# Kernel optimization log

Measured on AMD Instinct MI355X. Metric: run time of the kernel, lower is better.

The kernel has to match this reference:

```python
import jax, jax.numpy as jnp
import numpy as np

N_STATIC = 20
N_DYNAMIC = 10
INPUT_DIM = N_STATIC + N_DYNAMIC * 9 + 8  # 118
EMBED = 128
HIDDEN = 1536
HIDDEN2 = 1024
OUT = 128
T = 2048


def setup_inputs() -> dict:
    key = jax.random.key(0)
    ks = jax.random.split(key, 20)
    s = lambda i, shape: jax.random.normal(ks[i], shape, dtype=jnp.float32) * 0.02
    inp = {
        "inputVecs": jax.random.normal(ks[0], (T, INPUT_DIM), dtype=jnp.float32),
        # init_hidden(): randn(num_layers, 1, hidden_dim) -> stored as [2, H]
        "h0": jax.random.normal(ks[1], (2, HIDDEN), dtype=jnp.float32),
        "c0": jax.random.normal(ks[2], (2, HIDDEN), dtype=jnp.float32),
        # LSTM layer 0 (input = INPUT_DIM + EMBED)
        "W_ih0": s(3, (4 * HIDDEN, INPUT_DIM + EMBED)),
        "W_hh0": s(4, (4 * HIDDEN, HIDDEN)),
        "b_ih0": s(5, (4 * HIDDEN,)),
        "b_hh0": s(6, (4 * HIDDEN,)),
        # LSTM layer 1
        "W_ih1": s(7, (4 * HIDDEN, HIDDEN)),
        "W_hh1": s(8, (4 * HIDDEN, HIDDEN)),
        "b_ih1": s(9, (4 * HIDDEN,)),
        "b_hh1": s(10, (4 * HIDDEN,)),
        # hiddenLinear: hidden_dim -> hidden2
        "W_hl": s(11, (HIDDEN2, HIDDEN)),
        "b_hl": s(12, (HIDDEN2,)),
        # linear: hidden2 -> output_dim
        "W_out": s(13, (OUT, HIDDEN2)),
        "b_out": s(14, (OUT,)),
        # map: output_dim -> embed_size
        "W_map": s(15, (EMBED, OUT)),
        "b_map": s(16, (EMBED,)),
    }
    return inp


def _lstm_cell(x, h, c, W_ih, W_hh, b_ih, b_hh):
    # torch gate order: i, f, g, o
    gates = W_ih @ x + b_ih + W_hh @ h + b_hh
    i, f, g, o = jnp.split(gates, 4)
    i = jax.nn.sigmoid(i)
    f = jax.nn.sigmoid(f)
    g = jnp.tanh(g)
    o = jax.nn.sigmoid(o)
    c_new = f * c + i * g
    h_new = o * jnp.tanh(c_new)
    return h_new, c_new


def reference(inputVecs, h0, c0, W_ih0, W_hh0, b_ih0, b_hh0,
              W_ih1, W_hh1, b_ih1, b_hh1,
              W_hl, b_hl, W_out, b_out, W_map, b_map):
    embed0 = jnp.zeros((EMBED,), dtype=inputVecs.dtype)

    def step(carry, x):
        h, c, emb = carry  # h,c: [2, H]; emb: [EMBED]
        xt = jnp.concatenate([x, emb])
        h0n, c0n = _lstm_cell(xt, h[0], c[0], W_ih0, W_hh0, b_ih0, b_hh0)
        h1n, c1n = _lstm_cell(h0n, h[1], c[1], W_ih1, W_hh1, b_ih1, b_hh1)
        # dropout p=0 -> identity; two stacked linears (no nonlinearity, faithful)
        y = W_out @ (W_hl @ h1n + b_hl) + b_out
        y = jax.nn.softmax(y)
        emb_new = W_map @ y + b_map
        return (jnp.stack([h0n, h1n]), jnp.stack([c0n, c1n]), emb_new), y

    _, outputs = jax.lax.scan(step, (h0, c0, embed0), inputVecs)
    return outputs  # [T, OUT]
```

## Files before the change

kernel.cpp:

```cpp
#include <hip/hip_runtime.h>
#include <math.h>
#include <stdint.h>

#define T_STEPS 2048
#define XDIM 118
#define EMBD 128
#define HD 1536
#define NA 96
#define NB 128
#define NBLK (NA + NB + 1)

#define SMEM_BYTES 160608

typedef uint32_t u32x4 __attribute__((ext_vector_type(4)));

struct Params {
  const float *x, *h0in, *c0in;
  const float *Wih0, *Whh0, *bih0, *bhh0;
  const float *Wih1, *Whh1, *bih1, *bhh1;
  const float *Whl, *bhl, *Wout, *bout;
  const float *Wfold;
  float *PRE, *Wc, *bc;
  uint4 *h0rec, *h1rec, *partrec, *yrec;
  float *out;
};

__device__ __forceinline__ float bf_lo(uint32_t u){ return __uint_as_float(u << 16); }
__device__ __forceinline__ float bf_hi(uint32_t u){ return __uint_as_float(u & 0xffff0000u); }
__device__ __forceinline__ uint32_t packbf(float a, float b){
  uint32_t ua = __float_as_uint(a), ub = __float_as_uint(b);
  ua = (ua + 0x7fffu + ((ua >> 16) & 1u)) >> 16;
  ub = (ub + 0x7fffu + ((ub >> 16) & 1u)) & 0xffff0000u;
  return (ua & 0xffffu) | ub;
}
__device__ __forceinline__ float sigm(float x){ return 1.f / (1.f + __expf(-x)); }

__device__ __forceinline__ u32x4 poll_rec(const uint4* p, uint32_t tag){
  u32x4 r; uint32_t n = 0;
  while (1){
    asm volatile("global_load_dwordx4 %0, %1, off sc0 sc1\n\ts_waitcnt vmcnt(0)"
                 : "=v"(r) : "v"(p) : "memory");
    if (r[2] >= tag) break;
    __builtin_amdgcn_s_sleep(2);
    if (++n > 2000000u) break;
  }
  return r;
}
__device__ __forceinline__ u32x4 rec_issue(const uint4* p){
  u32x4 r;
  asm volatile("global_load_dwordx4 %0, %1, off sc0 sc1" : "=v"(r) : "v"(p) : "memory");
  return r;
}
__device__ __forceinline__ void st_rec(uint4* p, float a, float b, uint32_t tag){
  u32x4 v; v[0] = __float_as_uint(a); v[1] = __float_as_uint(b); v[2] = tag; v[3] = 0u;
  asm volatile("global_store_dwordx4 %0, %1, off sc0 sc1" :: "v"(p), "v"(v) : "memory");
}

__device__ __forceinline__ float asrc(const Params& P, int r, int k){
  if (k < HD) return P.Whh0[(size_t)r * HD + k];
  return P.Wih0[(size_t)r * (XDIM + EMBD) + XDIM + (k - HD)];
}
__device__ void run_A(const Params& P, int bid, uint32_t* smem){
  const int tid = threadIdx.x;
  const int w = tid >> 6, l = tid & 63;
  const int O = bid * 16 + w;
  float* xv = (float*)smem;
  uint2* wl2 = (uint2*)(smem + 1664);
  float* h0loc = (float*)(smem + 18048);
  uint32_t wr[4][8];
  uint32_t wry[4];
#pragma unroll
  for (int g = 0; g < 4; ++g){
    int r = g * HD + O;
#pragma unroll
    for (int p = 0; p < 8; ++p)
      wr[g][p] = packbf(asrc(P, r, 128 * p + 2 * l), asrc(P, r, 128 * p + 2 * l + 1));
#pragma unroll
    for (int q = 0; q < 2; ++q){
      uint2 u;
      u.x = packbf(asrc(P, r, 128 * (8 + 2 * q) + 2 * l), asrc(P, r, 128 * (8 + 2 * q) + 2 * l + 1));
      u.y = packbf(asrc(P, r, 128 * (9 + 2 * q) + 2 * l), asrc(P, r, 128 * (9 + 2 * q) + 2 * l + 1));
      wl2[(q * 4 + g) * 1024 + tid] = u;
    }
    wry[g] = packbf(P.Wfold[(size_t)r * 128 + 2 * l], P.Wfold[(size_t)r * 128 + 2 * l + 1]);
  }
  float cst = P.c0in[O];
  __syncthreads();
  for (int t = 0; t < T_STEPS; ++t){
    const float* pre = P.PRE + (size_t)t * 6144;
    float q0 = pre[O], q1 = pre[HD + O], q2 = pre[2 * HD + O], q3 = pre[3 * HD + O];
    if (tid < 768){
      u32x4 r = poll_rec(P.h0rec + ((t & 1) ^ 1) * 768 + tid, (uint32_t)t);
      xv[2 * tid] = __uint_as_float(r[0]);
      xv[2 * tid + 1] = __uint_as_float(r[1]);
    }
    __syncthreads();
    float a0 = 0.f, a1 = 0.f, a2 = 0.f, a3 = 0.f;
#pragma unroll
    for (int p = 0; p < 8; ++p){
      float2 x2 = *(const float2*)&xv[128 * p + 2 * l];
      uint32_t u0 = wr[0][p], u1 = wr[1][p], u2 = wr[2][p], u3 = wr[3][p];
      a0 += bf_lo(u0) * x2.x + bf_hi(u0) * x2.y;
      a1 += bf_lo(u1) * x2.x + bf_hi(u1) * x2.y;
      a2 += bf_lo(u2) * x2.x + bf_hi(u2) * x2.y;
      a3 += bf_lo(u3) * x2.x + bf_hi(u3) * x2.y;
    }
#pragma unroll
    for (int q = 0; q < 2; ++q){
      float2 xa = *(const float2*)&xv[128 * (8 + 2 * q) + 2 * l];
      float2 xb = *(const float2*)&xv[128 * (9 + 2 * q) + 2 * l];
      uint2 u0 = wl2[(q * 4 + 0) * 1024 + tid];
      uint2 u1 = wl2[(q * 4 + 1) * 1024 + tid];
      uint2 u2 = wl2[(q * 4 + 2) * 1024 + tid];
      uint2 u3 = wl2[(q * 4 + 3) * 1024 + tid];
      a0 += bf_lo(u0.x) * xa.x + bf_hi(u0.x) * xa.y + bf_lo(u0.y) * xb.x + bf_hi(u0.y) * xb.y;
      a1 += bf_lo(u1.x) * xa.x + bf_hi(u1.x) * xa.y + bf_lo(u1.y) * xb.x + bf_hi(u1.y) * xb.y;
      a2 += bf_lo(u2.x) * xa.x + bf_hi(u2.x) * xa.y + bf_lo(u2.y) * xb.x + bf_hi(u2.y) * xb.y;
      a3 += bf_lo(u3.x) * xa.x + bf_hi(u3.x) * xa.y + bf_lo(u3.y) * xb.x + bf_hi(u3.y) * xb.y;
    }
    if (t > 0){
      u32x4 r = poll_rec(P.yrec + ((t & 1) ^ 1) * 64 + l, (uint32_t)t);
      float y0 = __uint_as_float(r[0]), y1 = __uint_as_float(r[1]);
      a0 += bf_lo(wry[0]) * y0 + bf_hi(wry[0]) * y1;
      a1 += bf_lo(wry[1]) * y0 + bf_hi(wry[1]) * y1;
      a2 += bf_lo(wry[2]) * y0 + bf_hi(wry[2]) * y1;
      a3 += bf_lo(wry[3]) * y0 + bf_hi(wry[3]) * y1;
    }
#pragma unroll
    for (int m = 1; m < 64; m <<= 1){
      a0 += __shfl_xor(a0, m, 64);
      a1 += __shfl_xor(a1, m, 64);
      a2 += __shfl_xor(a2, m, 64);
      a3 += __shfl_xor(a3, m, 64);
    }
    float gi = sigm(a0 + q0);
    float gf = sigm(a1 + q1);
    float gg = tanhf(a2 + q2);
    float go = sigm(a3 + q3);
    cst = gf * cst + gi * gg;
    float hn = go * tanhf(cst);
    if (l == 0) h0loc[w] = hn;
    __syncthreads();
    if (tid < 8)
      st_rec(P.h0rec + (t & 1) * 768 + bid * 8 + tid,
             h0loc[2 * tid], h0loc[2 * tid + 1], (uint32_t)(t + 1));
  }
}

__device__ __forceinline__ float bsrc(const Params& P, int r, int k){
  if (k < HD) return P.Wih1[(size_t)r * HD + k];
  return P.Whh1[(size_t)r * HD + (k - HD)];
}
__device__ void run_B(const Params& P, int bidb, uint32_t* smem){
  const int tid = threadIdx.x;
  const int w = tid >> 6, l = tid & 63;
  const int base = bidb * 12;
  float* xv = (float*)smem;
  uint2* wl2 = (uint2*)(smem + 3072);
  float* g1 = (float*)(smem + 39936);
  float* c1 = (float*)(smem + 39984);
  float* h1loc = (float*)(smem + 40008);
  float* plds = (float*)(smem + 40020);
  uint32_t wr[3][12];
  float bias[3];
#pragma unroll
  for (int jj = 0; jj < 3; ++jj){
    int idx = 3 * w + jj;
    int g = idx / 12, o = idx % 12;
    int r = g * HD + base + o;
    bias[jj] = P.bih1[r] + P.bhh1[r];
#pragma unroll
    for (int p = 0; p < 12; ++p)
      wr[jj][p] = packbf(bsrc(P, r, 128 * p + 2 * l), bsrc(P, r, 128 * p + 2 * l + 1));
#pragma unroll
    for (int q = 0; q < 6; ++q){
      uint2 u;
      u.x = packbf(bsrc(P, r, 128 * (12 + 2 * q) + 2 * l), bsrc(P, r, 128 * (12 + 2 * q) + 2 * l + 1));
      u.y = packbf(bsrc(P, r, 128 * (13 + 2 * q) + 2 * l), bsrc(P, r, 128 * (13 + 2 * q) + 2 * l + 1));
      wl2[(q * 3 + jj) * 1024 + tid] = u;
    }
  }
  const int jrow = tid >> 2, cpart = tid & 3;
  float wc0 = 0.f, wc1 = 0.f, wc2 = 0.f;
  if (tid < 512){
    const float* wcp = P.Wc + (size_t)jrow * HD + base + cpart * 3;
    wc0 = wcp[0]; wc1 = wcp[1]; wc2 = wcp[2];
  }
  if (tid < 12) c1[12 + tid] = P.c0in[HD + base + tid];
  __syncthreads();
  for (int t = 0; t < T_STEPS; ++t){
    if (tid < 768){
      u32x4 r = poll_rec(P.h1rec + ((t & 1) ^ 1) * 768 + tid, (uint32_t)t);
      xv[1536 + 2 * tid] = __uint_as_float(r[0]);
      xv[1537 + 2 * tid] = __uint_as_float(r[1]);
    }
    __syncthreads();
    float a0 = 0.f, a1 = 0.f, a2 = 0.f;
#pragma unroll
    for (int q = 0; q < 6; ++q){
      float2 xa = *(const float2*)&xv[128 * (12 + 2 * q) + 2 * l];
      float2 xb = *(const float2*)&xv[128 * (13 + 2 * q) + 2 * l];
      uint2 u0 = wl2[(q * 3 + 0) * 1024 + tid];
      uint2 u1 = wl2[(q * 3 + 1) * 1024 + tid];
      uint2 u2 = wl2[(q * 3 + 2) * 1024 + tid];
      a0 += bf_lo(u0.x) * xa.x + bf_hi(u0.x) * xa.y + bf_lo(u0.y) * xb.x + bf_hi(u0.y) * xb.y;
      a1 += bf_lo(u1.x) * xa.x + bf_hi(u1.x) * xa.y + bf_lo(u1.y) * xb.x + bf_hi(u1.y) * xb.y;
      a2 += bf_lo(u2.x) * xa.x + bf_hi(u2.x) * xa.y + bf_lo(u2.y) * xb.x + bf_hi(u2.y) * xb.y;
    }
    if (tid < 768){
      u32x4 r = poll_rec(P.h0rec + (t & 1) * 768 + tid, (uint32_t)(t + 1));
      xv[2 * tid] = __uint_as_float(r[0]);
      xv[2 * tid + 1] = __uint_as_float(r[1]);
    }
    __syncthreads();
#pragma unroll
    for (int p = 0; p < 12; ++p){
      float2 x2 = *(const float2*)&xv[128 * p + 2 * l];
      uint32_t u0 = wr[0][p], u1 = wr[1][p], u2 = wr[2][p];
      a0 += bf_lo(u0) * x2.x + bf_hi(u0) * x2.y;
      a1 += bf_lo(u1) * x2.x + bf_hi(u1) * x2.y;
      a2 += bf_lo(u2) * x2.x + bf_hi(u2) * x2.y;
    }
#pragma unroll
    for (int m = 1; m < 64; m <<= 1){
      a0 += __shfl_xor(a0, m, 64);
      a1 += __shfl_xor(a1, m, 64);
      a2 += __shfl_xor(a2, m, 64);
    }
    if (l == 0){
      g1[3 * w + 0] = a0 + bias[0];
      g1[3 * w + 1] = a1 + bias[1];
      g1[3 * w + 2] = a2 + bias[2];
    }
    __syncthreads();
    const int par = ((t & 1) ^ 1) * 12, cur = (t & 1) * 12;
    if (tid < 512){
      float h[3], cc[3];
#pragma unroll
      for (int ii = 0; ii < 3; ++ii){
        int o = cpart * 3 + ii;
        float gi = sigm(g1[o]);
        float gf = sigm(g1[12 + o]);
        float gg = tanhf(g1[24 + o]);
        float go = sigm(g1[36 + o]);
        float c = gf * c1[par + o] + gi * gg;
        cc[ii] = c;
        h[ii] = go * tanhf(c);
      }
      float pp = wc0 * h[0] + wc1 * h[1] + wc2 * h[2];
      pp += __shfl_xor(pp, 1, 64);
      pp += __shfl_xor(pp, 2, 64);
      if (cpart == 0) plds[jrow] = pp;
      if (jrow == 0){
#pragma unroll
        for (int ii = 0; ii < 3; ++ii){
          int o = cpart * 3 + ii;
          c1[cur + o] = cc[ii];
          h1loc[o] = h[ii];
        }
      }
    }
    __syncthreads();
    uint32_t tg = (uint32_t)(t + 1);
    if (tid < 6)
      st_rec(P.h1rec + (t & 1) * 768 + bidb * 6 + tid,
             h1loc[2 * tid], h1loc[2 * tid + 1], tg);
    else if (tid >= 64 && tid < 128){
      int r = tid - 64;
      st_rec(P.partrec + (size_t)(t & 1) * 8192 + bidb * 64 + r,
             plds[2 * r], plds[2 * r + 1], tg);
    }
  }
}

__device__ void run_C(const Params& P, uint32_t* smem){
  const int tid = threadIdx.x;
  float* partred = (float*)smem;
  float* bcs = (float*)(smem + 2048);
  const int w = tid >> 6, l = tid & 63;
  const int g8 = tid >> 6, j2 = tid & 63;
  if (tid < 128) bcs[tid] = P.bc[tid];
  __syncthreads();
  for (int t = 0; t < T_STEPS; ++t){
    const uint4* base = P.partrec + (size_t)(t & 1) * 8192;
    uint32_t tg = (uint32_t)(t + 1);
    u32x4 rec[8];
    uint32_t done = 0, n = 0;
    while (done != 0xFFu){
#pragma unroll
      for (int k = 0; k < 8; ++k)
        if (!(done & (1u << k))) rec[k] = rec_issue(base + (size_t)(8 * g8 + k) * 64 + j2);
      asm volatile("s_waitcnt vmcnt(0)" ::: "memory");
      __builtin_amdgcn_sched_barrier(0);
#pragma unroll
      for (int k = 0; k < 8; ++k)
        if (rec[k][2] >= tg) done |= (1u << k);
      if (done != 0xFFu){
        __builtin_amdgcn_s_sleep(2);
        if (++n > 2000000u) break;
      }
    }
    float s0 = 0.f, s1 = 0.f;
#pragma unroll
    for (int k = 0; k < 8; ++k){
      s0 += __uint_as_float(rec[k][0]);
      s1 += __uint_as_float(rec[k][1]);
    }
    partred[g8 * 128 + 2 * j2] = s0;
    partred[g8 * 128 + 2 * j2 + 1] = s1;
    __syncthreads();
    if (w == 0){
      float lt0 = bcs[2 * l], lt1 = bcs[2 * l + 1];
#pragma unroll
      for (int g = 0; g < 16; ++g){
        lt0 += partred[g * 128 + 2 * l];
        lt1 += partred[g * 128 + 2 * l + 1];
      }
      float m = fmaxf(lt0, lt1);
#pragma unroll
      for (int k = 1; k < 64; k <<= 1) m = fmaxf(m, __shfl_xor(m, k, 64));
      float e0 = __expf(lt0 - m), e1 = __expf(lt1 - m);
      float sd = e0 + e1;
#pragma unroll
      for (int k = 1; k < 64; k <<= 1) sd += __shfl_xor(sd, k, 64);
      float inv = 1.f / sd;
      float y0 = e0 * inv, y1 = e1 * inv;
      P.out[(size_t)t * 128 + 2 * l] = y0;
      P.out[(size_t)t * 128 + 2 * l + 1] = y1;
      st_rec(P.yrec + (t & 1) * 64 + l, y0, y1, tg);
    }
  }
}

__global__ __launch_bounds__(1024) void k_lstm(Params P){
  extern __shared__ __align__(16) uint32_t smem[];
  int bid = blockIdx.x;
  if (bid < NA) run_A(P, bid, smem);
  else if (bid < NA + NB) run_B(P, bid - NA, smem);
  else run_C(P, smem);
}

__global__ void k_init(const float* h0in, uint4* h0rec, uint4* h1rec,
                       uint4* partrec, uint4* yrec){
  int tid = threadIdx.x;
  for (int i = tid; i < 768; i += 256){
    uint4 r0; r0.x = __float_as_uint(h0in[2 * i]); r0.y = __float_as_uint(h0in[2 * i + 1]);
    r0.z = 0u; r0.w = 0u;
    h0rec[i] = r0; h0rec[768 + i] = r0;
    uint4 r1; r1.x = __float_as_uint(h0in[HD + 2 * i]); r1.y = __float_as_uint(h0in[HD + 2 * i + 1]);
    r1.z = 0u; r1.w = 0u;
    h1rec[i] = r1; h1rec[768 + i] = r1;
  }
  uint4 z; z.x = 0u; z.y = 0u; z.z = 0u; z.w = 0u;
  for (int i = tid; i < 16384; i += 256) partrec[i] = z;
  for (int i = tid; i < 128; i += 256) yrec[i] = z;
}

__global__ void k_fold(const float* Wih0, const float* Wmap, const float* bmap,
                       float* Wfold, float* bfold){
  __shared__ float we[64 * 128];
  int b = blockIdx.x, tid = threadIdx.x;
  int r0 = b * 64;
  for (int i = tid; i < 64 * 128; i += 256){
    int rr = i >> 7, e = i & 127;
    we[i] = Wih0[(size_t)(r0 + rr) * (XDIM + EMBD) + XDIM + e];
  }
  __syncthreads();
  int j = tid & 127, half = tid >> 7;
  float acc[32];
#pragma unroll
  for (int rr = 0; rr < 32; ++rr) acc[rr] = 0.f;
  for (int e = 0; e < 128; ++e){
    float wv = Wmap[(size_t)e * 128 + j];
#pragma unroll
    for (int rr = 0; rr < 32; ++rr) acc[rr] += we[(half * 32 + rr) * 128 + e] * wv;
  }
  for (int rr = 0; rr < 32; ++rr)
    Wfold[(size_t)(r0 + half * 32 + rr) * 128 + j] = acc[rr];
  if (tid < 64){
    float a = 0.f;
    for (int e = 0; e < 128; ++e) a += we[tid * 128 + e] * bmap[e];
    bfold[r0 + tid] = a;
  }
}

__global__ void k_pre(const float* x, const float* Wih0, const float* bih0, const float* bhh0,
                      const float* bfold, float* PRE){
  int tb = blockIdx.x >> 2;
  int rc = blockIdx.x & 3;
  int tid = threadIdx.x;
  __shared__ float xl[32 * XDIM];
  for (int i = tid; i < 32 * XDIM; i += 256){
    int tt = i / XDIM, k = i % XDIM;
    xl[i] = x[(size_t)(tb * 32 + tt) * XDIM + k];
  }
  __syncthreads();
  for (int rr = 0; rr < 6; ++rr){
    int r = rc * HD + rr * 256 + tid;
    float acc[32];
#pragma unroll
    for (int t = 0; t < 32; ++t) acc[t] = 0.f;
    const float* wrow = Wih0 + (size_t)r * (XDIM + EMBD);
    for (int k = 0; k < XDIM; ++k){
      float wv = wrow[k];
#pragma unroll
      for (int t = 0; t < 32; ++t) acc[t] += wv * xl[t * XDIM + k];
    }
    float bb = bih0[r] + bhh0[r];
    float bf = bfold[r];
    for (int t = 0; t < 32; ++t)
      PRE[(size_t)(tb * 32 + t) * 6144 + r] = acc[t] + bb + ((tb * 32 + t) > 0 ? bf : 0.f);
  }
}

__global__ void k_wc(const float* Whl, const float* Wout, const float* bhl, const float* bout,
                     float* Wc, float* bc){
  if (blockIdx.x == 96){
    int j = threadIdx.x;
    if (j < 128){
      float a = 0.f;
      for (int m = 0; m < 1024; ++m) a += Wout[(size_t)j * 1024 + m] * bhl[m];
      bc[j] = a + bout[j];
    }
    return;
  }
  int kt = blockIdx.x % 6, jt = blockIdx.x / 6;
  __shared__ float wo[8 * 1024];
  int tid = threadIdx.x;
  for (int i = tid; i < 8 * 1024; i += 256) wo[i] = Wout[(size_t)(jt * 8) * 1024 + i];
  __syncthreads();
  int k = kt * 256 + tid;
  float acc[8];
#pragma unroll
  for (int jj = 0; jj < 8; ++jj) acc[jj] = 0.f;
  for (int m = 0; m < 1024; ++m){
    float wl = Whl[(size_t)m * HD + k];
#pragma unroll
    for (int jj = 0; jj < 8; ++jj) acc[jj] += wo[jj * 1024 + m] * wl;
  }
#pragma unroll
  for (int jj = 0; jj < 8; ++jj) Wc[(size_t)(jt * 8 + jj) * HD + k] = acc[jj];
}

__global__ void k_sentinel(float* out){ out[0] = 1.0e6f; }

extern "C" void kernel_launch(void* const* d_in, const int* in_sizes, int n_in,
                              void* d_out, int out_size, void* d_ws, size_t ws_size,
                              hipStream_t stream){
  (void)in_sizes; (void)n_in; (void)out_size;
  const float* x    = (const float*)d_in[0];
  const float* h0in = (const float*)d_in[1];
  const float* c0in = (const float*)d_in[2];
  const float* Wih0 = (const float*)d_in[3];
  const float* Whh0 = (const float*)d_in[4];
  const float* bih0 = (const float*)d_in[5];
  const float* bhh0 = (const float*)d_in[6];
  const float* Wih1 = (const float*)d_in[7];
  const float* Whh1 = (const float*)d_in[8];
  const float* bih1 = (const float*)d_in[9];
  const float* bhh1 = (const float*)d_in[10];
  const float* Whl  = (const float*)d_in[11];
  const float* bhl  = (const float*)d_in[12];
  const float* Wout = (const float*)d_in[13];
  const float* bout = (const float*)d_in[14];
  const float* Wmap = (const float*)d_in[15];
  const float* bmap = (const float*)d_in[16];
  float* out = (float*)d_out;
  float* ws = (float*)d_ws;

  size_t off = 0;
  float* PRE    = ws + off; off += (size_t)T_STEPS * 6144;
  float* Wc     = ws + off; off += 128 * HD;
  float* bc     = ws + off; off += 128;
  float* Wfold  = ws + off; off += (size_t)6144 * 128;
  float* bfold  = ws + off; off += 6144;
  off = (off + 3) & ~(size_t)3;
  uint4* h0rec   = (uint4*)(ws + off); off += 2 * 768 * 4;
  uint4* h1rec   = (uint4*)(ws + off); off += 2 * 768 * 4;
  uint4* partrec = (uint4*)(ws + off); off += 2 * 8192 * 4;
  uint4* yrec    = (uint4*)(ws + off); off += 2 * 64 * 4;

  if (ws_size < off * sizeof(float) + 1024){
    hipLaunchKernelGGL(k_sentinel, dim3(1), dim3(1), 0, stream, out);
    return;
  }

  (void)hipFuncSetAttribute(reinterpret_cast<const void*>(k_lstm),
                            hipFuncAttributeMaxDynamicSharedMemorySize, SMEM_BYTES);

  hipLaunchKernelGGL(k_init, dim3(1), dim3(256), 0, stream, h0in, h0rec, h1rec, partrec, yrec);
  hipLaunchKernelGGL(k_fold, dim3(96), dim3(256), 0, stream, Wih0, Wmap, bmap, Wfold, bfold);
  hipLaunchKernelGGL(k_pre, dim3(256), dim3(256), 0, stream, x, Wih0, bih0, bhh0, bfold, PRE);
  hipLaunchKernelGGL(k_wc, dim3(97), dim3(256), 0, stream, Whl, Wout, bhl, bout, Wc, bc);

  Params P;
  P.x = x; P.h0in = h0in; P.c0in = c0in;
  P.Wih0 = Wih0; P.Whh0 = Whh0; P.bih0 = bih0; P.bhh0 = bhh0;
  P.Wih1 = Wih1; P.Whh1 = Whh1; P.bih1 = bih1; P.bhh1 = bhh1;
  P.Whl = Whl; P.bhl = bhl; P.Wout = Wout; P.bout = bout;
  P.Wfold = Wfold;
  P.PRE = PRE; P.Wc = Wc; P.bc = bc;
  P.h0rec = h0rec; P.h1rec = h1rec; P.partrec = partrec; P.yrec = yrec;
  P.out = out;

  hipLaunchKernelGGL(k_lstm, dim3(NBLK), dim3(1024), SMEM_BYTES, stream, P);
}
```

Measured before the change: 27.81 ms.

## Replace per-record tagged polling with per-block tag flags and packed data buffers

Cross-block communication changes from tagged records, where every 16-byte record carries a tag and many threads poll, to dense float4 data buffers plus one tag word per producer block. A single wavefront polls all producer tags and releases the rest of the block through an LDS flag, then the data is read once without polling. Producers write data, wait for the stores to complete, then publish a tag. This cuts the global polling traffic and doubles the payload per record, at the cost of an extra store-ordering wait and LDS spin barriers. The memory-ordering correctness between data and tag visibility is the main risk.

```diff
diff --git a/kernel.cpp b/kernel.cpp
--- a/kernel.cpp
+++ b/kernel.cpp
@@ -13,6 +13,7 @@
 #define SMEM_BYTES 160608
 
 typedef uint32_t u32x4 __attribute__((ext_vector_type(4)));
+typedef uint32_t u32x2 __attribute__((ext_vector_type(2)));
 
 struct Params {
   const float *x, *h0in, *c0in;
@@ -21,7 +22,8 @@
   const float *Whl, *bhl, *Wout, *bout;
   const float *Wfold;
   float *PRE, *Wc, *bc;
-  uint4 *h0rec, *h1rec, *partrec, *yrec;
+  uint4 *h0dat, *h1dat, *partdat, *yrec;
+  uint32_t *atag, *btag;
   float *out;
 };
 
@@ -35,25 +37,69 @@
 }
 __device__ __forceinline__ float sigm(float x){ return 1.f / (1.f + __expf(-x)); }
 
+__device__ __forceinline__ u32x4 ld_rec(const uint4* p){
+  u32x4 r;
+  asm volatile("global_load_dwordx4 %0, %1, off sc0 sc1\n\ts_waitcnt vmcnt(0)"
+               : "=v"(r) : "v"(p) : "memory");
+  return r;
+}
+__device__ __forceinline__ void st_rec4(uint4* p, float4 d){
+  u32x4 v; v[0] = __float_as_uint(d.x); v[1] = __float_as_uint(d.y);
+  v[2] = __float_as_uint(d.z); v[3] = __float_as_uint(d.w);
+  asm volatile("global_store_dwordx4 %0, %1, off sc0 sc1" :: "v"(p), "v"(v) : "memory");
+}
+__device__ __forceinline__ void st_tag(uint32_t* p, uint32_t v){
+  asm volatile("global_store_dword %0, %1, off sc0 sc1" :: "v"(p), "v"(v) : "memory");
+}
 __device__ __forceinline__ u32x4 poll_rec(const uint4* p, uint32_t tag){
   u32x4 r; uint32_t n = 0;
   while (1){
     asm volatile("global_load_dwordx4 %0, %1, off sc0 sc1\n\ts_waitcnt vmcnt(0)"
                  : "=v"(r) : "v"(p) : "memory");
     if (r[2] >= tag) break;
-    __builtin_amdgcn_s_sleep(2);
+    __builtin_amdgcn_s_sleep(1);
     if (++n > 2000000u) break;
   }
   return r;
 }
-__device__ __forceinline__ u32x4 rec_issue(const uint4* p){
-  u32x4 r;
-  asm volatile("global_load_dwordx4 %0, %1, off sc0 sc1" : "=v"(r) : "v"(p) : "memory");
-  return r;
-}
-__device__ __forceinline__ void st_rec(uint4* p, float a, float b, uint32_t tag){
-  u32x4 v; v[0] = __float_as_uint(a); v[1] = __float_as_uint(b); v[2] = tag; v[3] = 0u;
-  asm volatile("global_store_dwordx4 %0, %1, off sc0 sc1" :: "v"(p), "v"(v) : "memory");
+__device__ __forceinline__ void poll_tags96(const uint32_t* tag, int l, uint32_t tgt){
+  uint32_t n = 0;
+  while (1){
+    uint32_t v0, v1;
+    asm volatile("global_load_dword %0, %2, off sc0 sc1\n\t"
+                 "global_load_dword %1, %3, off sc0 sc1\n\t"
+                 "s_waitcnt vmcnt(0)"
+                 : "=v"(v0), "=v"(v1)
+                 : "v"(tag + 4 * l), "v"(tag + 4 * (64 + (l & 31))) : "memory");
+    bool ok = (v0 >= tgt) && (l >= 32 || v1 >= tgt);
+    if (__all(ok)) break;
+    __builtin_amdgcn_s_sleep(1);
+    if (++n > 2000000u) break;
+  }
+}
+__device__ __forceinline__ void poll_tags128(const uint32_t* tag, int l, uint32_t tgt){
+  uint32_t n = 0;
+  while (1){
+    uint32_t v0, v1;
+    asm volatile("global_load_dword %0, %2, off sc0 sc1\n\t"
+                 "global_load_dword %1, %3, off sc0 sc1\n\t"
+                 "s_waitcnt vmcnt(0)"
+                 : "=v"(v0), "=v"(v1)
+                 : "v"(tag + 4 * l), "v"(tag + 4 * (64 + l)) : "memory");
+    if (__all(v0 >= tgt && v1 >= tgt)) break;
+    __builtin_amdgcn_s_sleep(1);
+    if (++n > 2000000u) break;
+  }
+}
+__device__ __forceinline__ void lds_set(volatile uint32_t* f, uint32_t v){
+  asm volatile("" ::: "memory");
+  *f = v;
+  asm volatile("" ::: "memory");
+}
+__device__ __forceinline__ void lds_wait(volatile uint32_t* f, uint32_t tgt){
+  uint32_t n = 0;
+  while (*f < tgt){ if (++n > 1000000000u) break; }
+  asm volatile("" ::: "memory");
 }
 
 __device__ __forceinline__ float asrc(const Params& P, int r, int k){
@@ -65,8 +111,10 @@
   const int w = tid >> 6, l = tid & 63;
   const int O = bid * 16 + w;
   float* xv = (float*)smem;
+  float* ybc = (float*)smem + 1536;
   uint2* wl2 = (uint2*)(smem + 1664);
   float* h0loc = (float*)(smem + 18048);
+  volatile uint32_t* flg = smem + 18064;
   uint32_t wr[4][8];
   uint32_t wry[4];
 #pragma unroll
@@ -85,14 +133,22 @@
     wry[g] = packbf(P.Wfold[(size_t)r * 128 + 2 * l], P.Wfold[(size_t)r * 128 + 2 * l + 1]);
   }
   float cst = P.c0in[O];
+  if (tid < 2) flg[tid] = 0u;
   __syncthreads();
   for (int t = 0; t < T_STEPS; ++t){
     const float* pre = P.PRE + (size_t)t * 6144;
     float q0 = pre[O], q1 = pre[HD + O], q2 = pre[2 * HD + O], q3 = pre[3 * HD + O];
-    if (tid < 768){
-      u32x4 r = poll_rec(P.h0rec + ((t & 1) ^ 1) * 768 + tid, (uint32_t)t);
-      xv[2 * tid] = __uint_as_float(r[0]);
-      xv[2 * tid + 1] = __uint_as_float(r[1]);
+    if (w == 0){
+      if (t > 0) poll_tags96(P.atag, l, (uint32_t)t);
+      lds_set(flg + 0, (uint32_t)t);
+    } else if (w < 6){
+      lds_wait(flg + 0, (uint32_t)t);
+    }
+    if (tid < 384){
+      u32x4 r = ld_rec(P.h0dat + ((t & 1) ^ 1) * 384 + tid);
+      float4 f; f.x = __uint_as_float(r[0]); f.y = __uint_as_float(r[1]);
+      f.z = __uint_as_float(r[2]); f.w = __uint_as_float(r[3]);
+      *(float4*)&xv[4 * tid] = f;
     }
     __syncthreads();
     float a0 = 0.f, a1 = 0.f, a2 = 0.f, a3 = 0.f;
@@ -119,8 +175,15 @@
       a3 += bf_lo(u3.x) * xa.x + bf_hi(u3.x) * xa.y + bf_lo(u3.y) * xb.x + bf_hi(u3.y) * xb.y;
     }
     if (t > 0){
-      u32x4 r = poll_rec(P.yrec + ((t & 1) ^ 1) * 64 + l, (uint32_t)t);
-      float y0 = __uint_as_float(r[0]), y1 = __uint_as_float(r[1]);
+      if (w == 0){
+        u32x4 r = poll_rec(P.yrec + ((t & 1) ^ 1) * 64 + l, (uint32_t)t);
+        ybc[2 * l] = __uint_as_float(r[0]);
+        ybc[2 * l + 1] = __uint_as_float(r[1]);
+        lds_set(flg + 1, (uint32_t)t);
+      } else {
+        lds_wait(flg + 1, (uint32_t)t);
+      }
+      float y0 = ybc[2 * l], y1 = ybc[2 * l + 1];
       a0 += bf_lo(wry[0]) * y0 + bf_hi(wry[0]) * y1;
       a1 += bf_lo(wry[1]) * y0 + bf_hi(wry[1]) * y1;
       a2 += bf_lo(wry[2]) * y0 + bf_hi(wry[2]) * y1;
@@ -141,9 +204,12 @@
     float hn = go * tanhf(cst);
     if (l == 0) h0loc[w] = hn;
     __syncthreads();
-    if (tid < 8)
-      st_rec(P.h0rec + (t & 1) * 768 + bid * 8 + tid,
-             h0loc[2 * tid], h0loc[2 * tid + 1], (uint32_t)(t + 1));
+    if (w == 0){
+      if (l < 4) st_rec4(P.h0dat + (t & 1) * 384 + bid * 4 + l,
+                         *(const float4*)&h0loc[4 * l]);
+      asm volatile("s_waitcnt vmcnt(0)" ::: "memory");
+      if (l == 0) st_tag(P.atag + 4 * bid, (uint32_t)(t + 1));
+    }
   }
 }
 
@@ -161,6 +227,7 @@
   float* c1 = (float*)(smem + 39984);
   float* h1loc = (float*)(smem + 40008);
   float* plds = (float*)(smem + 40020);
+  volatile uint32_t* flg = smem + 40148;
   uint32_t wr[3][12];
   float bias[3];
 #pragma unroll
@@ -187,12 +254,20 @@
     wc0 = wcp[0]; wc1 = wcp[1]; wc2 = wcp[2];
   }
   if (tid < 12) c1[12 + tid] = P.c0in[HD + base + tid];
+  if (tid < 2) flg[tid] = 0u;
   __syncthreads();
   for (int t = 0; t < T_STEPS; ++t){
-    if (tid < 768){
-      u32x4 r = poll_rec(P.h1rec + ((t & 1) ^ 1) * 768 + tid, (uint32_t)t);
-      xv[1536 + 2 * tid] = __uint_as_float(r[0]);
-      xv[1537 + 2 * tid] = __uint_as_float(r[1]);
+    if (w == 0){
+      if (t > 0) poll_tags128(P.btag, l, (uint32_t)t);
+      lds_set(flg + 0, (uint32_t)t);
+    } else if (w < 6){
+      lds_wait(flg + 0, (uint32_t)t);
+    }
+    if (tid < 384){
+      u32x4 r = ld_rec(P.h1dat + ((t & 1) ^ 1) * 384 + tid);
+      float4 f; f.x = __uint_as_float(r[0]); f.y = __uint_as_float(r[1]);
+      f.z = __uint_as_float(r[2]); f.w = __uint_as_float(r[3]);
+      *(float4*)&xv[1536 + 4 * tid] = f;
     }
     __syncthreads();
     float a0 = 0.f, a1 = 0.f, a2 = 0.f;
@@ -207,10 +282,17 @@
       a1 += bf_lo(u1.x) * xa.x + bf_hi(u1.x) * xa.y + bf_lo(u1.y) * xb.x + bf_hi(u1.y) * xb.y;
       a2 += bf_lo(u2.x) * xa.x + bf_hi(u2.x) * xa.y + bf_lo(u2.y) * xb.x + bf_hi(u2.y) * xb.y;
     }
-    if (tid < 768){
-      u32x4 r = poll_rec(P.h0rec + (t & 1) * 768 + tid, (uint32_t)(t + 1));
-      xv[2 * tid] = __uint_as_float(r[0]);
-      xv[2 * tid + 1] = __uint_as_float(r[1]);
+    if (w == 0){
+      poll_tags96(P.atag, l, (uint32_t)(t + 1));
+      lds_set(flg + 1, (uint32_t)(t + 1));
+    } else if (w < 6){
+      lds_wait(flg + 1, (uint32_t)(t + 1));
+    }
+    if (tid < 384){
+      u32x4 r = ld_rec(P.h0dat + (t & 1) * 384 + tid);
+      float4 f; f.x = __uint_as_float(r[0]); f.y = __uint_as_float(r[1]);
+      f.z = __uint_as_float(r[2]); f.w = __uint_as_float(r[3]);
+      *(float4*)&xv[4 * tid] = f;
     }
     __syncthreads();
 #pragma unroll
@@ -261,14 +343,17 @@
       }
     }
     __syncthreads();
-    uint32_t tg = (uint32_t)(t + 1);
-    if (tid < 6)
-      st_rec(P.h1rec + (t & 1) * 768 + bidb * 6 + tid,
-             h1loc[2 * tid], h1loc[2 * tid + 1], tg);
-    else if (tid >= 64 && tid < 128){
-      int r = tid - 64;
-      st_rec(P.partrec + (size_t)(t & 1) * 8192 + bidb * 64 + r,
-             plds[2 * r], plds[2 * r + 1], tg);
+    if (w == 1){
+      if (l < 32){
+        st_rec4(P.partdat + ((size_t)(t & 1) * 128 + bidb) * 32 + l,
+                *(const float4*)&plds[4 * l]);
+      } else if (l < 35){
+        int r = l - 32;
+        st_rec4(P.h1dat + (t & 1) * 384 + bidb * 3 + r,
+                *(const float4*)&h1loc[4 * r]);
+      }
+      asm volatile("s_waitcnt vmcnt(0)" ::: "memory");
+      if (l == 0) st_tag(P.btag + 4 * bidb, (uint32_t)(t + 1));
     }
   }
 }
@@ -276,43 +361,44 @@
 __device__ void run_C(const Params& P, uint32_t* smem){
   const int tid = threadIdx.x;
   float* partred = (float*)smem;
-  float* bcs = (float*)(smem + 2048);
+  float* bcs = (float*)(smem + 4096);
+  volatile uint32_t* flg = smem + 4224;
   const int w = tid >> 6, l = tid & 63;
-  const int g8 = tid >> 6, j2 = tid & 63;
+  const int s = tid & 31, bg = tid >> 5;
   if (tid < 128) bcs[tid] = P.bc[tid];
+  if (tid == 0) flg[0] = 0u;
   __syncthreads();
   for (int t = 0; t < T_STEPS; ++t){
-    const uint4* base = P.partrec + (size_t)(t & 1) * 8192;
     uint32_t tg = (uint32_t)(t + 1);
-    u32x4 rec[8];
-    uint32_t done = 0, n = 0;
-    while (done != 0xFFu){
-#pragma unroll
-      for (int k = 0; k < 8; ++k)
-        if (!(done & (1u << k))) rec[k] = rec_issue(base + (size_t)(8 * g8 + k) * 64 + j2);
-      asm volatile("s_waitcnt vmcnt(0)" ::: "memory");
-      __builtin_amdgcn_sched_barrier(0);
-#pragma unroll
-      for (int k = 0; k < 8; ++k)
-        if (rec[k][2] >= tg) done |= (1u << k);
-      if (done != 0xFFu){
-        __builtin_amdgcn_s_sleep(2);
-        if (++n > 2000000u) break;
-      }
-    }
-    float s0 = 0.f, s1 = 0.f;
-#pragma unroll
-    for (int k = 0; k < 8; ++k){
-      s0 += __uint_as_float(rec[k][0]);
-      s1 += __uint_as_float(rec[k][1]);
-    }
-    partred[g8 * 128 + 2 * j2] = s0;
-    partred[g8 * 128 + 2 * j2 + 1] = s1;
+    if (w == 0){
+      poll_tags128(P.btag, l, tg);
+      lds_set(flg, tg);
+    } else {
+      lds_wait(flg, tg);
+    }
+    {
+      const uint4* pb = P.partdat + ((size_t)(t & 1) * 128 + 4 * bg) * 32 + s;
+      u32x4 r0, r1, r2, r3;
+      asm volatile(
+        "global_load_dwordx4 %0, %4, off sc0 sc1\n\t"
+        "global_load_dwordx4 %1, %5, off sc0 sc1\n\t"
+        "global_load_dwordx4 %2, %6, off sc0 sc1\n\t"
+        "global_load_dwordx4 %3, %7, off sc0 sc1\n\t"
+        "s_waitcnt vmcnt(0)"
+        : "=v"(r0), "=v"(r1), "=v"(r2), "=v"(r3)
+        : "v"(pb), "v"(pb + 32), "v"(pb + 64), "v"(pb + 96) : "memory");
+      float4 acc;
+      acc.x = __uint_as_float(r0[0]) + __uint_as_float(r1[0]) + __uint_as_float(r2[0]) + __uint_as_float(r3[0]);
+      acc.y = __uint_as_float(r0[1]) + __uint_as_float(r1[1]) + __uint_as_float(r2[1]) + __uint_as_float(r3[1]);
+      acc.z = __uint_as_float(r0[2]) + __uint_as_float(r1[2]) + __uint_as_float(r2[2]) + __uint_as_float(r3[2]);
+      acc.w = __uint_as_float(r0[3]) + __uint_as_float(r1[3]) + __uint_as_float(r2[3]) + __uint_as_float(r3[3]);
+      *(float4*)&partred[bg * 128 + 4 * s] = acc;
+    }
     __syncthreads();
     if (w == 0){
       float lt0 = bcs[2 * l], lt1 = bcs[2 * l + 1];
 #pragma unroll
-      for (int g = 0; g < 16; ++g){
+      for (int g = 0; g < 32; ++g){
         lt0 += partred[g * 128 + 2 * l];
         lt1 += partred[g * 128 + 2 * l + 1];
       }
@@ -327,7 +413,9 @@
       float y0 = e0 * inv, y1 = e1 * inv;
       P.out[(size_t)t * 128 + 2 * l] = y0;
       P.out[(size_t)t * 128 + 2 * l + 1] = y1;
-      st_rec(P.yrec + (t & 1) * 64 + l, y0, y1, tg);
+      u32x4 v; v[0] = __float_as_uint(y0); v[1] = __float_as_uint(y1); v[2] = tg; v[3] = 0u;
+      uint4* yp = P.yrec + (t & 1) * 64 + l;
+      asm volatile("global_store_dwordx4 %0, %1, off sc0 sc1" :: "v"(yp), "v"(v) : "memory");
     }
   }
 }
@@ -340,20 +428,23 @@
   else run_C(P, smem);
 }
 
-__global__ void k_init(const float* h0in, uint4* h0rec, uint4* h1rec,
-                       uint4* partrec, uint4* yrec){
+__global__ void k_init(const float* h0in, uint4* h0dat, uint4* h1dat, uint4* yrec,
+                       uint32_t* atag, uint32_t* btag){
   int tid = threadIdx.x;
   for (int i = tid; i < 768; i += 256){
-    uint4 r0; r0.x = __float_as_uint(h0in[2 * i]); r0.y = __float_as_uint(h0in[2 * i + 1]);
-    r0.z = 0u; r0.w = 0u;
-    h0rec[i] = r0; h0rec[768 + i] = r0;
-    uint4 r1; r1.x = __float_as_uint(h0in[HD + 2 * i]); r1.y = __float_as_uint(h0in[HD + 2 * i + 1]);
-    r1.z = 0u; r1.w = 0u;
-    h1rec[i] = r1; h1rec[768 + i] = r1;
+    int r = i % 384;
+    uint4 v0, v1;
+    v0.x = __float_as_uint(h0in[4 * r]);     v0.y = __float_as_uint(h0in[4 * r + 1]);
+    v0.z = __float_as_uint(h0in[4 * r + 2]); v0.w = __float_as_uint(h0in[4 * r + 3]);
+    h0dat[i] = v0;
+    v1.x = __float_as_uint(h0in[HD + 4 * r]);     v1.y = __float_as_uint(h0in[HD + 4 * r + 1]);
+    v1.z = __float_as_uint(h0in[HD + 4 * r + 2]); v1.w = __float_as_uint(h0in[HD + 4 * r + 3]);
+    h1dat[i] = v1;
   }
   uint4 z; z.x = 0u; z.y = 0u; z.z = 0u; z.w = 0u;
-  for (int i = tid; i < 16384; i += 256) partrec[i] = z;
   for (int i = tid; i < 128; i += 256) yrec[i] = z;
+  for (int i = tid; i < 96 * 4; i += 256) atag[i] = 0u;
+  for (int i = tid; i < 128 * 4; i += 256) btag[i] = 0u;
 }
 
 __global__ void k_fold(const float* Wih0, const float* Wmap, const float* bmap,
@@ -474,11 +565,14 @@
   float* bc     = ws + off; off += 128;
   float* Wfold  = ws + off; off += (size_t)6144 * 128;
   float* bfold  = ws + off; off += 6144;
-  off = (off + 3) & ~(size_t)3;
-  uint4* h0rec   = (uint4*)(ws + off); off += 2 * 768 * 4;
-  uint4* h1rec   = (uint4*)(ws + off); off += 2 * 768 * 4;
-  uint4* partrec = (uint4*)(ws + off); off += 2 * 8192 * 4;
-  uint4* yrec    = (uint4*)(ws + off); off += 2 * 64 * 4;
+  off = (off + 31) & ~(size_t)31;
+  uint4* h0dat   = (uint4*)(ws + off); off += 768 * 4;
+  uint4* h1dat   = (uint4*)(ws + off); off += 768 * 4;
+  uint4* partdat = (uint4*)(ws + off); off += 2 * 128 * 32 * 4;
+  uint4* yrec    = (uint4*)(ws + off); off += 128 * 4;
+  uint32_t* atag = (uint32_t*)(ws + off); off += 96 * 4;
+  off = (off + 31) & ~(size_t)31;
+  uint32_t* btag = (uint32_t*)(ws + off); off += 128 * 4;
 
   if (ws_size < off * sizeof(float) + 1024){
     hipLaunchKernelGGL(k_sentinel, dim3(1), dim3(1), 0, stream, out);
@@ -488,7 +582,7 @@
   (void)hipFuncSetAttribute(reinterpret_cast<const void*>(k_lstm),
                             hipFuncAttributeMaxDynamicSharedMemorySize, SMEM_BYTES);
 
-  hipLaunchKernelGGL(k_init, dim3(1), dim3(256), 0, stream, h0in, h0rec, h1rec, partrec, yrec);
+  hipLaunchKernelGGL(k_init, dim3(1), dim3(256), 0, stream, h0in, h0dat, h1dat, yrec, atag, btag);
   hipLaunchKernelGGL(k_fold, dim3(96), dim3(256), 0, stream, Wih0, Wmap, bmap, Wfold, bfold);
   hipLaunchKernelGGL(k_pre, dim3(256), dim3(256), 0, stream, x, Wih0, bih0, bhh0, bfold, PRE);
   hipLaunchKernelGGL(k_wc, dim3(97), dim3(256), 0, stream, Whl, Wout, bhl, bout, Wc, bc);
@@ -500,7 +594,8 @@
   P.Whl = Whl; P.bhl = bhl; P.Wout = Wout; P.bout = bout;
   P.Wfold = Wfold;
   P.PRE = PRE; P.Wc = Wc; P.bc = bc;
-  P.h0rec = h0rec; P.h1rec = h1rec; P.partrec = partrec; P.yrec = yrec;
+  P.h0dat = h0dat; P.h1dat = h1dat; P.partdat = partdat; P.yrec = yrec;
+  P.atag = atag; P.btag = btag;
   P.out = out;
 
   hipLaunchKernelGGL(k_lstm, dim3(NBLK), dim3(1024), SMEM_BYTES, stream, P);
```

Result: slower. 37.61 ms (+35.3%).

## Publish one hidden value per record to drop per-step block barriers

Applied to the files above, without the earlier changes.

Each wave now writes its own hidden-state record (one float plus tag) straight to global memory, instead of gathering values in LDS behind a __syncthreads and storing pairs. Consumers poll two records per thread with both loads issued before a single wait. Layer-A's input buffer is double-buffered by step parity so the trailing barrier can be removed safely. Partial sums are also stored directly from shuffled registers. This shortens the cross-block critical path each timestep, at the cost of twice as many records to poll and more small stores.

```diff
diff --git a/kernel.cpp b/kernel.cpp
--- a/kernel.cpp
+++ b/kernel.cpp
@@ -46,6 +46,21 @@
   }
   return r;
 }
+__device__ __forceinline__ void poll2(const uint4* p0, const uint4* p1, uint32_t tag,
+                                      float* d0, float* d1){
+  u32x4 a, b; uint32_t n = 0;
+  while (1){
+    asm volatile("global_load_dwordx4 %0, %2, off sc0 sc1\n\t"
+                 "global_load_dwordx4 %1, %3, off sc0 sc1\n\t"
+                 "s_waitcnt vmcnt(0)"
+                 : "=v"(a), "=v"(b) : "v"(p0), "v"(p1) : "memory");
+    if (a[2] >= tag && b[2] >= tag) break;
+    __builtin_amdgcn_s_sleep(2);
+    if (++n > 2000000u) break;
+  }
+  *d0 = __uint_as_float(a[0]);
+  *d1 = __uint_as_float(b[0]);
+}
 __device__ __forceinline__ u32x4 rec_issue(const uint4* p){
   u32x4 r;
   asm volatile("global_load_dwordx4 %0, %1, off sc0 sc1" : "=v"(r) : "v"(p) : "memory");
@@ -64,9 +79,7 @@
   const int tid = threadIdx.x;
   const int w = tid >> 6, l = tid & 63;
   const int O = bid * 16 + w;
-  float* xv = (float*)smem;
-  uint2* wl2 = (uint2*)(smem + 1664);
-  float* h0loc = (float*)(smem + 18048);
+  uint2* wl2 = (uint2*)(smem + 3072);
   uint32_t wr[4][8];
   uint32_t wry[4];
 #pragma unroll
@@ -89,10 +102,10 @@
   for (int t = 0; t < T_STEPS; ++t){
     const float* pre = P.PRE + (size_t)t * 6144;
     float q0 = pre[O], q1 = pre[HD + O], q2 = pre[2 * HD + O], q3 = pre[3 * HD + O];
+    float* xv = (float*)smem + (t & 1) * 1536;
     if (tid < 768){
-      u32x4 r = poll_rec(P.h0rec + ((t & 1) ^ 1) * 768 + tid, (uint32_t)t);
-      xv[2 * tid] = __uint_as_float(r[0]);
-      xv[2 * tid + 1] = __uint_as_float(r[1]);
+      const uint4* p = P.h0rec + ((t & 1) ^ 1) * 1536 + 2 * tid;
+      poll2(p, p + 1, (uint32_t)t, &xv[2 * tid], &xv[2 * tid + 1]);
     }
     __syncthreads();
     float a0 = 0.f, a1 = 0.f, a2 = 0.f, a3 = 0.f;
@@ -139,11 +152,7 @@
     float go = sigm(a3 + q3);
     cst = gf * cst + gi * gg;
     float hn = go * tanhf(cst);
-    if (l == 0) h0loc[w] = hn;
-    __syncthreads();
-    if (tid < 8)
-      st_rec(P.h0rec + (t & 1) * 768 + bid * 8 + tid,
-             h0loc[2 * tid], h0loc[2 * tid + 1], (uint32_t)(t + 1));
+    if (l == 0) st_rec(P.h0rec + (t & 1) * 1536 + O, hn, 0.f, (uint32_t)(t + 1));
   }
 }
 
@@ -159,8 +168,6 @@
   uint2* wl2 = (uint2*)(smem + 3072);
   float* g1 = (float*)(smem + 39936);
   float* c1 = (float*)(smem + 39984);
-  float* h1loc = (float*)(smem + 40008);
-  float* plds = (float*)(smem + 40020);
   uint32_t wr[3][12];
   float bias[3];
 #pragma unroll
@@ -190,9 +197,8 @@
   __syncthreads();
   for (int t = 0; t < T_STEPS; ++t){
     if (tid < 768){
-      u32x4 r = poll_rec(P.h1rec + ((t & 1) ^ 1) * 768 + tid, (uint32_t)t);
-      xv[1536 + 2 * tid] = __uint_as_float(r[0]);
-      xv[1537 + 2 * tid] = __uint_as_float(r[1]);
+      const uint4* p = P.h1rec + ((t & 1) ^ 1) * 1536 + 2 * tid;
+      poll2(p, p + 1, (uint32_t)t, &xv[1536 + 2 * tid], &xv[1537 + 2 * tid]);
     }
     __syncthreads();
     float a0 = 0.f, a1 = 0.f, a2 = 0.f;
@@ -208,9 +214,8 @@
       a2 += bf_lo(u2.x) * xa.x + bf_hi(u2.x) * xa.y + bf_lo(u2.y) * xb.x + bf_hi(u2.y) * xb.y;
     }
     if (tid < 768){
-      u32x4 r = poll_rec(P.h0rec + (t & 1) * 768 + tid, (uint32_t)(t + 1));
-      xv[2 * tid] = __uint_as_float(r[0]);
-      xv[2 * tid + 1] = __uint_as_float(r[1]);
+      const uint4* p = P.h0rec + (t & 1) * 1536 + 2 * tid;
+      poll2(p, p + 1, (uint32_t)(t + 1), &xv[2 * tid], &xv[2 * tid + 1]);
     }
     __syncthreads();
 #pragma unroll
@@ -234,6 +239,7 @@
     }
     __syncthreads();
     const int par = ((t & 1) ^ 1) * 12, cur = (t & 1) * 12;
+    uint32_t tg = (uint32_t)(t + 1);
     if (tid < 512){
       float h[3], cc[3];
 #pragma unroll
@@ -250,25 +256,17 @@
       float pp = wc0 * h[0] + wc1 * h[1] + wc2 * h[2];
       pp += __shfl_xor(pp, 1, 64);
       pp += __shfl_xor(pp, 2, 64);
-      if (cpart == 0) plds[jrow] = pp;
+      float pp2 = __shfl_xor(pp, 4, 64);
+      if ((tid & 7) == 0)
+        st_rec(P.partrec + (size_t)(t & 1) * 8192 + bidb * 64 + (tid >> 3), pp, pp2, tg);
       if (jrow == 0){
 #pragma unroll
         for (int ii = 0; ii < 3; ++ii){
           int o = cpart * 3 + ii;
           c1[cur + o] = cc[ii];
-          h1loc[o] = h[ii];
+          st_rec(P.h1rec + (t & 1) * 1536 + base + o, h[ii], 0.f, tg);
         }
       }
-    }
-    __syncthreads();
-    uint32_t tg = (uint32_t)(t + 1);
-    if (tid < 6)
-      st_rec(P.h1rec + (t & 1) * 768 + bidb * 6 + tid,
-             h1loc[2 * tid], h1loc[2 * tid + 1], tg);
-    else if (tid >= 64 && tid < 128){
-      int r = tid - 64;
-      st_rec(P.partrec + (size_t)(t & 1) * 8192 + bidb * 64 + r,
-             plds[2 * r], plds[2 * r + 1], tg);
     }
   }
 }
@@ -343,13 +341,11 @@
 __global__ void k_init(const float* h0in, uint4* h0rec, uint4* h1rec,
                        uint4* partrec, uint4* yrec){
   int tid = threadIdx.x;
-  for (int i = tid; i < 768; i += 256){
-    uint4 r0; r0.x = __float_as_uint(h0in[2 * i]); r0.y = __float_as_uint(h0in[2 * i + 1]);
-    r0.z = 0u; r0.w = 0u;
-    h0rec[i] = r0; h0rec[768 + i] = r0;
-    uint4 r1; r1.x = __float_as_uint(h0in[HD + 2 * i]); r1.y = __float_as_uint(h0in[HD + 2 * i + 1]);
-    r1.z = 0u; r1.w = 0u;
-    h1rec[i] = r1; h1rec[768 + i] = r1;
+  for (int i = tid; i < 1536; i += 256){
+    uint4 r0; r0.x = __float_as_uint(h0in[i]); r0.y = 0u; r0.z = 0u; r0.w = 0u;
+    h0rec[i] = r0; h0rec[1536 + i] = r0;
+    uint4 r1; r1.x = __float_as_uint(h0in[HD + i]); r1.y = 0u; r1.z = 0u; r1.w = 0u;
+    h1rec[i] = r1; h1rec[1536 + i] = r1;
   }
   uint4 z; z.x = 0u; z.y = 0u; z.z = 0u; z.w = 0u;
   for (int i = tid; i < 16384; i += 256) partrec[i] = z;
@@ -475,8 +471,8 @@
   float* Wfold  = ws + off; off += (size_t)6144 * 128;
   float* bfold  = ws + off; off += 6144;
   off = (off + 3) & ~(size_t)3;
-  uint4* h0rec   = (uint4*)(ws + off); off += 2 * 768 * 4;
-  uint4* h1rec   = (uint4*)(ws + off); off += 2 * 768 * 4;
+  uint4* h0rec   = (uint4*)(ws + off); off += 2 * 1536 * 4;
+  uint4* h1rec   = (uint4*)(ws + off); off += 2 * 1536 * 4;
   uint4* partrec = (uint4*)(ws + off); off += 2 * 8192 * 4;
   uint4* yrec    = (uint4*)(ws + off); off += 2 * 64 * 4;
 
```

Result: slower. 44.24 ms (+59.1%).
